# Performance work log

Hardware: AMD Instinct MI355X
Metric: run time of the kernel (lower is better)

Reference implementation:

```python
import jax, jax.numpy as jnp
import numpy as np

DELTA = -5.0
DECAY = 0.95
EPS = 1e-05


def setup_inputs() -> dict:
    key = jax.random.key(0)
    k1, k2, k3 = jax.random.split(key, 3)
    N, K, D = 16384, 1024, 256
    z = jax.random.normal(k1, (N, D), dtype=jnp.float32)
    centroids = jax.random.normal(k2, (K, D), dtype=jnp.float32)
    ema_w = jax.random.normal(k3, (K, D), dtype=jnp.float32)
    ema_cluster_size = jnp.ones((K,), dtype=jnp.float32)
    return {"z": z, "centroids": centroids, "ema_w": ema_w,
            "ema_cluster_size": ema_cluster_size}


def reference(z, centroids, ema_w, ema_cluster_size):
    # z: [N, D]; centroids/ema_w: [K, D]; ema_cluster_size: [K]
    K = centroids.shape[0]
    # squared L2 distances via ||z||^2 - 2 z.C^T + ||c||^2 (same math as
    # sum((z[:,None,:]-C)**2, -1), without the (N,K,D) intermediate)
    z_sq = jnp.sum(z * z, axis=1, keepdims=True)          # [N, 1]
    c_sq = jnp.sum(centroids * centroids, axis=1)         # [K]
    z_dist = z_sq - 2.0 * (z @ centroids.T) + c_sq        # [N, K]
    gamma = jax.nn.softmax(DELTA * z_dist, axis=1)        # [N, K]
    idx = jnp.argmax(gamma, axis=1)                       # [N] int
    # recons = one_hot(idx) @ centroids == gather
    recons = centroids[idx]                               # [N, D]
    # --- EMA codebook update (training branch), expressed purely ---
    counts = jnp.zeros((K,), dtype=z.dtype).at[idx].add(jnp.ones((), z.dtype))
    new_cs = ema_cluster_size * DECAY + (1.0 - DECAY) * counts
    n = jnp.sum(new_cs)
    new_cs = (new_cs + EPS) / (n + K * EPS) * n
    dw = jax.ops.segment_sum(z, idx, num_segments=K)      # == Idx.T @ z, [K, D]
    new_w = ema_w * DECAY + (1.0 - DECAY) * dw
    new_centroids = new_w / new_cs[:, None]
    # straight-through estimator
    recons = z + jax.lax.stop_gradient(recons - z)
    return recons, gamma, new_centroids
```

## Files before the change

### kernel.cpp

```cpp
#include <hip/hip_runtime.h>
#include <hip/hip_bf16.h>


#define DECAY 0.95f
#define OMD   0.05f
#define EPSV  1e-5f

using f32x4  = __attribute__((ext_vector_type(4))) float;
using bf16x8 = __attribute__((ext_vector_type(8))) __bf16;

typedef __attribute__((address_space(3))) unsigned int       lds_uint;
typedef const __attribute__((address_space(1))) unsigned int glb_uint;

__device__ __forceinline__ void gload16(const void* g, const void* l) {
  __builtin_amdgcn_global_load_lds((glb_uint*)(unsigned long long)g,
                                   (lds_uint*)(unsigned int)(unsigned long long)l,
                                   16, 0, 0);
}

__device__ __forceinline__ unsigned short f2bf(float f) {
  unsigned int u = __float_as_uint(f);
  unsigned int r = (u + 0x7FFFu + ((u >> 16) & 1u)) >> 16;
  return (unsigned short)r;
}
__device__ __forceinline__ float bf2f(unsigned short s) {
  return __uint_as_float(((unsigned int)s) << 16);
}

__global__ __launch_bounds__(256) void convert_hilo(const float* __restrict__ src,
                                                    unsigned short* __restrict__ hi,
                                                    unsigned short* __restrict__ lo,
                                                    int total8) {
  const int i = blockIdx.x * 256 + threadIdx.x;
  if (i >= total8) return;
  const float4 a = ((const float4*)src)[2 * i];
  const float4 b = ((const float4*)src)[2 * i + 1];
  float f[8] = {a.x, a.y, a.z, a.w, b.x, b.y, b.z, b.w};
  union { unsigned short u[8]; uint4 v; } H, L;
#pragma unroll
  for (int j = 0; j < 8; ++j) {
    H.u[j] = f2bf(f[j]);
    L.u[j] = f2bf(f[j] - bf2f(H.u[j]));
  }
  ((uint4*)hi)[i] = H.v;
  ((uint4*)lo)[i] = L.v;
}

__global__ __launch_bounds__(64) void csq_kernel(const float* __restrict__ cent,
                                                 float* __restrict__ csq) {
  const int k = blockIdx.x;
  const int t = threadIdx.x;
  const float4 v = ((const float4*)(cent + (size_t)k * 256))[t];
  float s = v.x * v.x + v.y * v.y + v.z * v.z + v.w * v.w;
#pragma unroll
  for (int off = 32; off; off >>= 1) s += __shfl_down(s, off);
  if (t == 0) csq[k] = s;
}

__global__ __launch_bounds__(256, 2) void dist_gemm_mfma(
    const unsigned short* __restrict__ zh, const unsigned short* __restrict__ zl,
    const unsigned short* __restrict__ ch, const unsigned short* __restrict__ cl,
    const float* __restrict__ csq, float* __restrict__ dist) {
  __shared__ unsigned short lds[4][128 * 64];

  const int tid  = threadIdx.x;
  const int lane = tid & 63;
  const int w    = tid >> 6;

  const int bid = blockIdx.x;
  const int lin = (bid & 7) * 128 + (bid >> 3);
  const int m0  = (lin >> 3) * 128;
  const int n0  = (lin & 7) * 128;

  const int wm0 = (w >> 1) * 64;
  const int wn0 = (w & 1) * 64;

  f32x4 acc[4][4];
#pragma unroll
  for (int i = 0; i < 4; ++i)
#pragma unroll
    for (int j = 0; j < 4; ++j) acc[i][j] = (f32x4){0.f, 0.f, 0.f, 0.f};

  const int srow = lane >> 3;
  const int scb  = lane & 7;

  for (int d0 = 0; d0 < 256; d0 += 64) {
    __syncthreads();
#pragma unroll
    for (int j = 0; j < 4; ++j) {
      const int r0    = w * 32 + j * 8;
      const int row   = r0 + srow;
      const int chunk = scb ^ (row & 7);
      const size_t go = (size_t)(d0 + chunk * 8);
      gload16(zh + (size_t)(m0 + row) * 256 + go, &lds[0][r0 * 64]);
      gload16(zl + (size_t)(m0 + row) * 256 + go, &lds[1][r0 * 64]);
      gload16(ch + (size_t)(n0 + row) * 256 + go, &lds[2][r0 * 64]);
      gload16(cl + (size_t)(n0 + row) * 256 + go, &lds[3][r0 * 64]);
    }
    __syncthreads();
#pragma unroll
    for (int s = 0; s < 2; ++s) {
      bf16x8 ah[4], al[4], bh[4], bl[4];
      const int kg = s * 4 + (lane >> 4);
#pragma unroll
      for (int f = 0; f < 4; ++f) {
        const int ra = wm0 + f * 16 + (lane & 15);
        const int ca = kg ^ (ra & 7);
        ah[f] = *(const bf16x8*)&lds[0][ra * 64 + ca * 8];
        al[f] = *(const bf16x8*)&lds[1][ra * 64 + ca * 8];
        const int rb = wn0 + f * 16 + (lane & 15);
        const int cb = kg ^ (rb & 7);
        bh[f] = *(const bf16x8*)&lds[2][rb * 64 + cb * 8];
        bl[f] = *(const bf16x8*)&lds[3][rb * 64 + cb * 8];
      }
#pragma unroll
      for (int fm = 0; fm < 4; ++fm)
#pragma unroll
        for (int fn = 0; fn < 4; ++fn) {
          acc[fm][fn] = __builtin_amdgcn_mfma_f32_16x16x32_bf16(ah[fm], bh[fn], acc[fm][fn], 0, 0, 0);
          acc[fm][fn] = __builtin_amdgcn_mfma_f32_16x16x32_bf16(ah[fm], bl[fn], acc[fm][fn], 0, 0, 0);
          acc[fm][fn] = __builtin_amdgcn_mfma_f32_16x16x32_bf16(al[fm], bh[fn], acc[fm][fn], 0, 0, 0);
        }
    }
  }

#pragma unroll
  for (int fn = 0; fn < 4; ++fn) {
    const int col = n0 + wn0 + fn * 16 + (lane & 15);
    const float cq = csq[col];
#pragma unroll
    for (int fm = 0; fm < 4; ++fm) {
      const int row = m0 + wm0 + fm * 16 + ((lane >> 4) << 2);
#pragma unroll
      for (int r = 0; r < 4; ++r)
        dist[(size_t)(row + r) * 1024 + col] = cq - 2.0f * acc[fm][fn][r];
    }
  }
}

__global__ __launch_bounds__(256) void row_softmax(const float* __restrict__ z,
                                                   const float* __restrict__ cent,
                                                   float* __restrict__ gamma,
                                                   float* __restrict__ recons,
                                                   float* __restrict__ dw,
                                                   float* __restrict__ counts,
                                                   int K) {
  const int n = blockIdx.x;
  const int t = threadIdx.x;
  float* row = gamma + (size_t)n * K;
  const float4 s = ((const float4*)row)[t];

  float mv = s.x; int mi = 4 * t;
  if (s.y < mv) { mv = s.y; mi = 4 * t + 1; }
  if (s.z < mv) { mv = s.z; mi = 4 * t + 2; }
  if (s.w < mv) { mv = s.w; mi = 4 * t + 3; }

#pragma unroll
  for (int off = 32; off; off >>= 1) {
    const float ov = __shfl_down(mv, off);
    const int   oi = __shfl_down(mi, off);
    if (ov < mv || (ov == mv && oi < mi)) { mv = ov; mi = oi; }
  }

  __shared__ float wv[4];
  __shared__ int   wi[4];
  __shared__ float fmin_s;
  __shared__ int   fidx_s;
  __shared__ float fsum_s;
  const int wave = t >> 6;
  if ((t & 63) == 0) { wv[wave] = mv; wi[wave] = mi; }
  __syncthreads();
  if (t == 0) {
    float bv = wv[0]; int bi = wi[0];
#pragma unroll
    for (int wq = 1; wq < 4; ++wq)
      if (wv[wq] < bv || (wv[wq] == bv && wi[wq] < bi)) { bv = wv[wq]; bi = wi[wq]; }
    fmin_s = bv; fidx_s = bi;
  }
  __syncthreads();

  const float bm = fmin_s;
  const float e0 = __expf(-5.0f * (s.x - bm));
  const float e1 = __expf(-5.0f * (s.y - bm));
  const float e2 = __expf(-5.0f * (s.z - bm));
  const float e3 = __expf(-5.0f * (s.w - bm));
  float ls = e0 + e1 + e2 + e3;
#pragma unroll
  for (int off = 32; off; off >>= 1) ls += __shfl_down(ls, off);
  if ((t & 63) == 0) wv[wave] = ls;
  __syncthreads();
  if (t == 0) fsum_s = wv[0] + wv[1] + wv[2] + wv[3];
  __syncthreads();

  const float inv = 1.0f / fsum_s;
  float4 g;
  g.x = e0 * inv; g.y = e1 * inv; g.z = e2 * inv; g.w = e3 * inv;
  ((float4*)row)[t] = g;

  const int idx = fidx_s;
  const float zv = z[(size_t)n * 256 + t];
  recons[(size_t)n * 256 + t] = cent[(size_t)idx * 256 + t];
  atomicAdd(&dw[(size_t)idx * 256 + t], zv);
  if (t == 0) atomicAdd(&counts[idx], 1.0f);
}

__global__ __launch_bounds__(1024) void finalize_cs(const float* __restrict__ ema_cs,
                                                    const float* __restrict__ counts,
                                                    float* __restrict__ newcs, int K) {
  const int t = threadIdx.x;
  const float v = ema_cs[t] * DECAY + OMD * counts[t];
  float sum = v;
#pragma unroll
  for (int off = 32; off; off >>= 1) sum += __shfl_down(sum, off);
  __shared__ float wsum[16];
  __shared__ float tot_s;
  if ((t & 63) == 0) wsum[t >> 6] = sum;
  __syncthreads();
  if (t == 0) {
    float a = 0.0f;
#pragma unroll
    for (int i = 0; i < 16; ++i) a += wsum[i];
    tot_s = a;
  }
  __syncthreads();
  const float n = tot_s;
  newcs[t] = (v + EPSV) / (n + (float)K * EPSV) * n;
}

__global__ __launch_bounds__(256) void finalize_centroids(const float* __restrict__ ema_w,
                                                          const float* __restrict__ dw,
                                                          const float* __restrict__ newcs,
                                                          float* __restrict__ outc,
                                                          int total) {
  const int i = blockIdx.x * 256 + threadIdx.x;
  if (i < total) {
    const int k = i >> 8;
    outc[i] = (ema_w[i] * DECAY + OMD * dw[i]) / newcs[k];
  }
}

extern "C" void kernel_launch(void* const* d_in, const int* in_sizes, int n_in,
                              void* d_out, int out_size, void* d_ws, size_t ws_size,
                              hipStream_t stream) {
  const float* z      = (const float*)d_in[0];
  const float* cent   = (const float*)d_in[1];
  const float* ema_w  = (const float*)d_in[2];
  const float* ema_cs = (const float*)d_in[3];

  const int K = in_sizes[3];
  const int D = in_sizes[1] / K;
  const int N = in_sizes[0] / D;

  float* out    = (float*)d_out;
  float* recons = out;
  float* gamma  = out + (size_t)N * D;
  float* outc   = gamma + (size_t)N * K;

  unsigned short* zh = (unsigned short*)recons;
  unsigned short* zl = zh + (size_t)N * D;
  unsigned short* chp = (unsigned short*)outc;
  unsigned short* clp = chp + (size_t)K * D;

  float* dw     = (float*)d_ws;
  float* counts = dw + (size_t)K * D;
  float* csq    = counts + K;
  float* newcs  = csq + K;

  hipMemsetAsync(dw, 0, (size_t)(K * D + K) * sizeof(float), stream);

  convert_hilo<<<(N * D / 8 + 255) / 256, 256, 0, stream>>>(z, zh, zl, N * D / 8);
  convert_hilo<<<(K * D / 8 + 255) / 256, 256, 0, stream>>>(cent, chp, clp, K * D / 8);

  csq_kernel<<<K, 64, 0, stream>>>(cent, csq);

  dist_gemm_mfma<<<(N / 128) * (K / 128), 256, 0, stream>>>(zh, zl, chp, clp, csq, gamma);

  row_softmax<<<N, 256, 0, stream>>>(z, cent, gamma, recons, dw, counts, K);

  finalize_cs<<<1, K, 0, stream>>>(ema_cs, counts, newcs, K);

  finalize_centroids<<<(K * D + 255) / 256, 256, 0, stream>>>(ema_w, dw, newcs, outc, K * D);
}
```

Baseline: 95.34 us.

## Fuse prep kernels and memset into one launch and merge finalize kernels

Merges the two hi/lo bf16 conversions, the centroid squared-norm computation, the workspace zeroing and a sum of ema_cluster_size into a single prep kernel dispatched by block index. The two finalize kernels collapse into one per-centroid kernel that computes the total count analytically as DECAY*sum(ema_cs)+OMD*N, since every row adds exactly one count. This removes several launches, a memset and a single-block serial kernel, at the cost of hardcoded sizes (block counts, K=1024, D=256).

```diff
diff --git a/kernel.cpp b/kernel.cpp
--- a/kernel.cpp
+++ b/kernel.cpp
@@ -27,34 +27,61 @@
   return __uint_as_float(((unsigned int)s) << 16);
 }
 
-__global__ __launch_bounds__(256) void convert_hilo(const float* __restrict__ src,
-                                                    unsigned short* __restrict__ hi,
-                                                    unsigned short* __restrict__ lo,
-                                                    int total8) {
-  const int i = blockIdx.x * 256 + threadIdx.x;
-  if (i >= total8) return;
-  const float4 a = ((const float4*)src)[2 * i];
-  const float4 b = ((const float4*)src)[2 * i + 1];
-  float f[8] = {a.x, a.y, a.z, a.w, b.x, b.y, b.z, b.w};
-  union { unsigned short u[8]; uint4 v; } H, L;
-#pragma unroll
-  for (int j = 0; j < 8; ++j) {
-    H.u[j] = f2bf(f[j]);
-    L.u[j] = f2bf(f[j] - bf2f(H.u[j]));
-  }
-  ((uint4*)hi)[i] = H.v;
-  ((uint4*)lo)[i] = L.v;
-}
-
-__global__ __launch_bounds__(64) void csq_kernel(const float* __restrict__ cent,
-                                                 float* __restrict__ csq) {
-  const int k = blockIdx.x;
-  const int t = threadIdx.x;
-  const float4 v = ((const float4*)(cent + (size_t)k * 256))[t];
-  float s = v.x * v.x + v.y * v.y + v.z * v.z + v.w * v.w;
-#pragma unroll
-  for (int off = 32; off; off >>= 1) s += __shfl_down(s, off);
-  if (t == 0) csq[k] = s;
+__global__ __launch_bounds__(256) void prep(const float* __restrict__ z,
+                                            const float* __restrict__ cent,
+                                            const float* __restrict__ ema_cs,
+                                            unsigned short* __restrict__ zh,
+                                            unsigned short* __restrict__ zl,
+                                            unsigned short* __restrict__ chp,
+                                            unsigned short* __restrict__ clp,
+                                            float* __restrict__ csq,
+                                            float* __restrict__ dwzero,
+                                            float* __restrict__ S) {
+  const int bid = blockIdx.x;
+  const int t   = threadIdx.x;
+  if (bid < 2048) {
+    const int i = bid * 256 + t;
+    const float4 a = ((const float4*)z)[2 * i];
+    const float4 b = ((const float4*)z)[2 * i + 1];
+    float f[8] = {a.x, a.y, a.z, a.w, b.x, b.y, b.z, b.w};
+    union { unsigned short u[8]; uint4 v; } H, L;
+#pragma unroll
+    for (int j = 0; j < 8; ++j) {
+      H.u[j] = f2bf(f[j]);
+      L.u[j] = f2bf(f[j] - bf2f(H.u[j]));
+    }
+    ((uint4*)zh)[i] = H.v;
+    ((uint4*)zl)[i] = L.v;
+  } else if (bid < 2176) {
+    const int i = (bid - 2048) * 256 + t;
+    const float4 a = ((const float4*)cent)[2 * i];
+    const float4 b = ((const float4*)cent)[2 * i + 1];
+    float f[8] = {a.x, a.y, a.z, a.w, b.x, b.y, b.z, b.w};
+    union { unsigned short u[8]; uint4 v; } H, L;
+    float ss = 0.f;
+#pragma unroll
+    for (int j = 0; j < 8; ++j) {
+      H.u[j] = f2bf(f[j]);
+      L.u[j] = f2bf(f[j] - bf2f(H.u[j]));
+      ss += f[j] * f[j];
+    }
+    ((uint4*)chp)[i] = H.v;
+    ((uint4*)clp)[i] = L.v;
+#pragma unroll
+    for (int off = 16; off; off >>= 1) ss += __shfl_down(ss, off, 32);
+    if ((t & 31) == 0) csq[(bid - 2048) * 8 + (t >> 5)] = ss;
+  } else if (bid < 2433) {
+    const int i = (bid - 2176) * 256 + t;
+    ((float4*)dwzero)[i] = (float4){0.f, 0.f, 0.f, 0.f};
+  } else {
+    float s = ema_cs[t] + ema_cs[t + 256] + ema_cs[t + 512] + ema_cs[t + 768];
+#pragma unroll
+    for (int off = 32; off; off >>= 1) s += __shfl_down(s, off);
+    __shared__ float wsum[4];
+    if ((t & 63) == 0) wsum[t >> 6] = s;
+    __syncthreads();
+    if (t == 0) S[0] = wsum[0] + wsum[1] + wsum[2] + wsum[3];
+  }
 }
 
 __global__ __launch_bounds__(256, 2) void dist_gemm_mfma(
@@ -204,39 +231,20 @@
   if (t == 0) atomicAdd(&counts[idx], 1.0f);
 }
 
-__global__ __launch_bounds__(1024) void finalize_cs(const float* __restrict__ ema_cs,
-                                                    const float* __restrict__ counts,
-                                                    float* __restrict__ newcs, int K) {
+__global__ __launch_bounds__(256) void finalize(const float* __restrict__ ema_w,
+                                                const float* __restrict__ ema_cs,
+                                                const float* __restrict__ counts,
+                                                const float* __restrict__ dw,
+                                                const float* __restrict__ S,
+                                                float* __restrict__ outc,
+                                                float fN) {
+  const int k = blockIdx.x;
   const int t = threadIdx.x;
-  const float v = ema_cs[t] * DECAY + OMD * counts[t];
-  float sum = v;
-#pragma unroll
-  for (int off = 32; off; off >>= 1) sum += __shfl_down(sum, off);
-  __shared__ float wsum[16];
-  __shared__ float tot_s;
-  if ((t & 63) == 0) wsum[t >> 6] = sum;
-  __syncthreads();
-  if (t == 0) {
-    float a = 0.0f;
-#pragma unroll
-    for (int i = 0; i < 16; ++i) a += wsum[i];
-    tot_s = a;
-  }
-  __syncthreads();
-  const float n = tot_s;
-  newcs[t] = (v + EPSV) / (n + (float)K * EPSV) * n;
-}
-
-__global__ __launch_bounds__(256) void finalize_centroids(const float* __restrict__ ema_w,
-                                                          const float* __restrict__ dw,
-                                                          const float* __restrict__ newcs,
-                                                          float* __restrict__ outc,
-                                                          int total) {
-  const int i = blockIdx.x * 256 + threadIdx.x;
-  if (i < total) {
-    const int k = i >> 8;
-    outc[i] = (ema_w[i] * DECAY + OMD * dw[i]) / newcs[k];
-  }
+  const float n   = DECAY * S[0] + OMD * fN;
+  const float v   = DECAY * ema_cs[k] + OMD * counts[k];
+  const float ncs = (v + EPSV) / (n + 1024.0f * EPSV) * n;
+  const size_t i  = (size_t)k * 256 + t;
+  outc[i] = (DECAY * ema_w[i] + OMD * dw[i]) / ncs;
 }
 
 extern "C" void kernel_launch(void* const* d_in, const int* in_sizes, int n_in,
@@ -256,28 +264,21 @@
   float* gamma  = out + (size_t)N * D;
   float* outc   = gamma + (size_t)N * K;
 
-  unsigned short* zh = (unsigned short*)recons;
-  unsigned short* zl = zh + (size_t)N * D;
+  unsigned short* zh  = (unsigned short*)recons;
+  unsigned short* zl  = zh + (size_t)N * D;
   unsigned short* chp = (unsigned short*)outc;
   unsigned short* clp = chp + (size_t)K * D;
 
   float* dw     = (float*)d_ws;
   float* counts = dw + (size_t)K * D;
   float* csq    = counts + K;
-  float* newcs  = csq + K;
-
-  hipMemsetAsync(dw, 0, (size_t)(K * D + K) * sizeof(float), stream);
-
-  convert_hilo<<<(N * D / 8 + 255) / 256, 256, 0, stream>>>(z, zh, zl, N * D / 8);
-  convert_hilo<<<(K * D / 8 + 255) / 256, 256, 0, stream>>>(cent, chp, clp, K * D / 8);
-
-  csq_kernel<<<K, 64, 0, stream>>>(cent, csq);
+  float* S      = csq + K;
+
+  prep<<<2434, 256, 0, stream>>>(z, cent, ema_cs, zh, zl, chp, clp, csq, dw, S);
 
   dist_gemm_mfma<<<(N / 128) * (K / 128), 256, 0, stream>>>(zh, zl, chp, clp, csq, gamma);
 
   row_softmax<<<N, 256, 0, stream>>>(z, cent, gamma, recons, dw, counts, K);
 
-  finalize_cs<<<1, K, 0, stream>>>(ema_cs, counts, newcs, K);
-
-  finalize_centroids<<<(K * D + 255) / 256, 256, 0, stream>>>(ema_w, dw, newcs, outc, K * D);
-}
+  finalize<<<K, 256, 0, stream>>>(ema_w, ema_cs, counts, dw, S, outc, (float)N);
+}
```

Result: faster. 84.11 us (-11.8%).
